# Kernel optimization log

Hardware: AMD Instinct MI355X
Metric: run time of the kernel (lower is better)

Reference implementation:

```python
import jax, jax.numpy as jnp
import numpy as np

LOG_VAR_Q = 0.0
TEMPERATURE = 0.5


def setup_inputs() -> dict:
    key = jax.random.key(0)
    k1, k2, k3 = jax.random.split(key, 3)
    bs, dim_z, W, H, K = 64, 64, 32, 32, 1024
    x = jax.random.normal(k1, (bs, dim_z, W, H), dtype=jnp.float32)
    codebook = jax.random.normal(k2, (K, dim_z), dtype=jnp.float32)
    log_var_q_scalar = jnp.asarray(0.0, dtype=jnp.float32)
    # pre-sampled standard Gumbel noise for the relaxed categorical
    u = jax.random.uniform(k3, (bs * W * H, K), dtype=jnp.float32,
                           minval=1e-6, maxval=1.0 - 1e-6)
    gumbel_noise = -jnp.log(-jnp.log(u))
    return {"x": x, "codebook": codebook,
            "log_var_q_scalar": log_var_q_scalar,
            "gumbel_noise": gumbel_noise}


def reference(x, codebook, log_var_q_scalar, gumbel_noise):
    bs, dim_z, W, H = x.shape
    # [bs, dim_z, W, H] -> [bs*W*H, dim_z]
    x_flat = jnp.transpose(x, (0, 2, 3, 1)).reshape(-1, dim_z)

    var_q = jnp.exp(jnp.asarray(LOG_VAR_Q, x.dtype)) + jnp.exp(log_var_q_scalar)
    precision_q = 1.0 / jnp.clip(var_q, 1e-10)
    w = 0.5 * precision_q  # scalar weight on squared distances

    sq_x = jnp.sum(x_flat * x_flat, axis=-1, keepdims=True)
    sq_c = jnp.sum(codebook * codebook, axis=-1)
    cross = jnp.einsum('nd,kd->nk', x_flat, codebook)
    logit = -w * (sq_x - 2.0 * cross + sq_c)

    log_probs = jax.nn.log_softmax(logit, axis=-1)
    probs = jnp.exp(log_probs)

    # gumbel-softmax relaxed one-hot encodings
    encodings = jax.nn.softmax((logit + gumbel_noise) / TEMPERATURE, axis=-1)

    quantized = jnp.einsum('nk,kd->nd', encodings, codebook)
    quantized = jnp.transpose(quantized.reshape(bs, W, H, dim_z), (0, 3, 1, 2))

    kld_discrete = jnp.sum(probs * log_probs) / bs
    kld_continuous = jnp.mean(jnp.sum(w * (x - quantized) ** 2, axis=(1, 2, 3)))
    return quantized, kld_discrete + kld_continuous
```

## Files before the change

### kernel.cpp

```cpp
#include <hip/hip_runtime.h>
#include <math.h>

#define K_CB 1024
#define D_Z  64
#define MT   16
#define NTOT 65536
#define NBLK (NTOT / MT)

typedef __attribute__((ext_vector_type(8))) short  s16x8;
typedef __attribute__((ext_vector_type(4))) short  s16x4;
typedef __attribute__((ext_vector_type(4))) float  f32x4;

#define WS_CB16  0
#define WS_CBT16 131072
#define WS_NWSQC 262144
#define WS_PART  266240

__device__ __forceinline__ unsigned short f2b(float f) {
  unsigned int u = __float_as_uint(f);
  u += 0x7fffu + ((u >> 16) & 1u);
  return (unsigned short)(u >> 16);
}

__global__ void vq_prep(const float* __restrict__ cb, const float* __restrict__ lvq,
                        unsigned char* __restrict__ wsb) {
  unsigned short* cb16  = (unsigned short*)(wsb + WS_CB16);
  unsigned short* cbT16 = (unsigned short*)(wsb + WS_CBT16);
  float* nwsqc = (float*)(wsb + WS_NWSQC);
  const float w = 0.5f / fmaxf(1.0f + __expf(lvq[0]), 1e-10f);
  const int tid = threadIdx.x;
  const int k  = blockIdx.x * 16 + (tid >> 4);
  const int d0 = (tid & 15) * 4;
  const f32x4 v = *(const f32x4*)(cb + k * D_Z + d0);
  s16x4 b4;
  #pragma unroll
  for (int i = 0; i < 4; i++) b4[i] = (short)f2b(v[i]);
  *(s16x4*)(cb16 + k * D_Z + d0) = b4;
  #pragma unroll
  for (int i = 0; i < 4; i++) cbT16[(d0 + i) * K_CB + k] = (unsigned short)b4[i];
  float s = v[0]*v[0] + v[1]*v[1] + v[2]*v[2] + v[3]*v[3];
  #pragma unroll
  for (int off = 1; off < 16; off <<= 1) s += __shfl_xor(s, off);
  if ((tid & 15) == 0) nwsqc[k] = -w * s;
}

__global__ __launch_bounds__(256, 3)
void vq_main(const float* __restrict__ x, const float* __restrict__ gum,
             const float* __restrict__ lvq, unsigned char* __restrict__ wsb,
             float* __restrict__ out) {
  __shared__ __align__(16) unsigned short xa[1024];
  __shared__ __align__(16) float xs[MT][68];
  __shared__ __align__(16) float sqcs[K_CB];
  __shared__ __align__(16) unsigned short es[MT][1032];
  __shared__ __align__(16) float pstat[4][MT][4];
  __shared__ __align__(16) float s2p[4][MT];
  __shared__ float kldrow[MT];
  __shared__ float wred[4];

  const int tid  = threadIdx.x;
  const int wv   = tid >> 6;
  const int lane = tid & 63;
  const int m16  = lane & 15;
  const int g    = lane >> 4;

  const int blk  = blockIdx.x;
  const int row0 = blk * MT;
  const int bidx = row0 >> 10;
  const int rem0 = row0 & 1023;

  const float w  = 0.5f / fmaxf(1.0f + __expf(lvq[0]), 1e-10f);
  const float w2 = 2.0f * w;

  const unsigned short* cb16  = (const unsigned short*)(wsb + WS_CB16);
  const unsigned short* cbT16 = (const unsigned short*)(wsb + WS_CBT16);
  const float* nwsqc = (const float*)(wsb + WS_NWSQC);

  {
    const int m = tid & 15, db = tid >> 4;
    #pragma unroll
    for (int i = 0; i < 4; i++) {
      const int d = db + 16 * i;
      const float v = x[((bidx * D_Z + d) << 10) + rem0 + m];
      xs[m][d] = v;
      xa[(d >> 5) * 512 + ((d >> 3) & 3) * 128 + m * 8 + (d & 7)] = f2b(v);
    }
    for (int k = tid; k < K_CB; k += 256) sqcs[k] = nwsqc[k];
  }
  __syncthreads();

  f32x4 acc[16];
  #pragma unroll
  for (int t = 0; t < 16; t++) acc[t] = (f32x4){0.f, 0.f, 0.f, 0.f};
  {
    const s16x8 xb0 = *(const s16x8*)(xa + g * 128 + m16 * 8);
    const s16x8 xb1 = *(const s16x8*)(xa + 512 + g * 128 + m16 * 8);
    const unsigned short* ap = cb16 + (wv * 256 + m16) * D_Z + g * 8;
    #pragma unroll
    for (int t = 0; t < 16; t++) {
      const s16x8 a0 = *(const s16x8*)(ap + t * 1024);
      const s16x8 a1 = *(const s16x8*)(ap + t * 1024 + 32);
      acc[t] = __builtin_amdgcn_mfma_f32_16x16x32_bf16(a0, xb0, acc[t], 0, 0, 0);
      acc[t] = __builtin_amdgcn_mfma_f32_16x16x32_bf16(a1, xb1, acc[t], 0, 0, 0);
    }
  }

  float m1 = -3.4e38f;
  #pragma unroll
  for (int t = 0; t < 16; t++) {
    const f32x4 sc = *(const f32x4*)&sqcs[wv * 256 + t * 16 + g * 4];
    #pragma unroll
    for (int r = 0; r < 4; r++) {
      acc[t][r] = fmaf(w2, acc[t][r], sc[r]);
      m1 = fmaxf(m1, acc[t][r]);
    }
  }
  m1 = fmaxf(m1, __shfl_xor(m1, 16));
  m1 = fmaxf(m1, __shfl_xor(m1, 32));
  float s1 = 0.f, Aa = 0.f;
  #pragma unroll
  for (int t = 0; t < 16; t++) {
    #pragma unroll
    for (int r = 0; r < 4; r++) {
      const float u = acc[t][r] - m1;
      const float e = __expf(u);
      s1 += e;
      Aa = fmaf(u, e, Aa);
    }
  }
  s1 += __shfl_xor(s1, 16); s1 += __shfl_xor(s1, 32);
  Aa += __shfl_xor(Aa, 16); Aa += __shfl_xor(Aa, 32);

  float m2 = -3.4e38f;
  const float* gp = gum + (row0 + m16) * K_CB + wv * 256 + g * 4;
  #pragma unroll
  for (int t = 0; t < 16; t++) {
    const f32x4 gv = __builtin_nontemporal_load((const f32x4*)(gp + t * 16));
    #pragma unroll
    for (int r = 0; r < 4; r++) {
      const float z = 2.0f * (acc[t][r] + gv[r]);
      acc[t][r] = z;
      m2 = fmaxf(m2, z);
    }
  }
  m2 = fmaxf(m2, __shfl_xor(m2, 16));
  m2 = fmaxf(m2, __shfl_xor(m2, 32));
  if (g == 0) {
    pstat[wv][m16][0] = m1; pstat[wv][m16][1] = s1;
    pstat[wv][m16][2] = Aa; pstat[wv][m16][3] = m2;
  }
  __syncthreads();

  float M2 = -3.4e38f;
  {
    float M1 = -3.4e38f;
    f32x4 pw[4];
    #pragma unroll
    for (int q = 0; q < 4; q++) {
      pw[q] = *(const f32x4*)&pstat[q][m16][0];
      M1 = fmaxf(M1, pw[q][0]);
      M2 = fmaxf(M2, pw[q][3]);
    }
    float s1g = 0.f, Ag = 0.f;
    #pragma unroll
    for (int q = 0; q < 4; q++) {
      const float dm = pw[q][0] - M1;
      const float c = __expf(dm);
      s1g += c * pw[q][1];
      Ag = fmaf(c, fmaf(dm, pw[q][1], pw[q][2]), Ag);
    }
    if (tid < 16) kldrow[m16] = Ag / s1g - __logf(s1g);
  }

  float s2 = 0.f;
  #pragma unroll
  for (int t = 0; t < 16; t++) {
    s16x4 ev;
    #pragma unroll
    for (int r = 0; r < 4; r++) {
      const float e = __expf(acc[t][r] - M2);
      s2 += e;
      ev[r] = (short)f2b(e);
    }
    *(s16x4*)&es[m16][wv * 256 + t * 16 + g * 4] = ev;
  }
  s2 += __shfl_xor(s2, 16); s2 += __shfl_xor(s2, 32);
  if (g == 0) s2p[wv][m16] = s2;
  __syncthreads();

  const float inv2 = 1.0f / (s2p[0][m16] + s2p[1][m16] + s2p[2][m16] + s2p[3][m16]);
  f32x4 qacc = (f32x4){0.f, 0.f, 0.f, 0.f};
  {
    const unsigned short* a2p = cbT16 + (wv * 16 + m16) * K_CB + g * 8;
    const unsigned short* b2p = &es[m16][g * 8];
    #pragma unroll
    for (int kc = 0; kc < 32; kc++) {
      const s16x8 a2 = *(const s16x8*)(a2p + kc * 32);
      const s16x8 b2 = *(const s16x8*)(b2p + kc * 32);
      qacc = __builtin_amdgcn_mfma_f32_16x16x32_bf16(a2, b2, qacc, 0, 0, 0);
    }
  }

  float kca = 0.f;
  #pragma unroll
  for (int r = 0; r < 4; r++) {
    const int d = wv * 16 + g * 4 + r;
    const float qv = qacc[r] * inv2;
    __builtin_nontemporal_store(qv, out + ((bidx * D_Z + d) << 10) + rem0 + m16);
    const float dx = xs[m16][d] - qv;
    kca = fmaf(dx, dx, kca);
  }
  #pragma unroll
  for (int off = 1; off < 64; off <<= 1) kca += __shfl_xor(kca, off);
  if (lane == 0) wred[wv] = kca;
  __syncthreads();
  if (tid == 0) {
    float tot = w * (wred[0] + wred[1] + wred[2] + wred[3]);
    #pragma unroll
    for (int i = 0; i < MT; i++) tot += kldrow[i];
    ((float*)(wsb + WS_PART))[blk] = tot;
  }
}

__global__ void vq_reduce(const unsigned char* __restrict__ wsb, float* __restrict__ out) {
  __shared__ float red[256];
  const float* part = (const float*)(wsb + WS_PART);
  const int t = threadIdx.x;
  float s = 0.f;
  for (int i = t; i < NBLK; i += 256) s += part[i];
  red[t] = s;
  __syncthreads();
  for (int st = 128; st > 0; st >>= 1) {
    if (t < st) red[t] += red[t + st];
    __syncthreads();
  }
  if (t == 0) out[NTOT * D_Z] = red[0] * (1.0f / 64.0f);
}

extern "C" void kernel_launch(void* const* d_in, const int* in_sizes, int n_in,
                              void* d_out, int out_size, void* d_ws, size_t ws_size,
                              hipStream_t stream) {
  const float* x   = (const float*)d_in[0];
  const float* cb  = (const float*)d_in[1];
  const float* lvq = (const float*)d_in[2];
  const float* gum = (const float*)d_in[3];
  float* out = (float*)d_out;
  unsigned char* wsb = (unsigned char*)d_ws;

  hipLaunchKernelGGL(vq_prep,   dim3(64),   dim3(256), 0, stream, cb, lvq, wsb);
  hipLaunchKernelGGL(vq_main,   dim3(NBLK), dim3(256), 0, stream, x, gum, lvq, wsb, out);
  hipLaunchKernelGGL(vq_reduce, dim3(1),    dim3(256), 0, stream, wsb, out);
}
```

Before: 179.1 us.

## Keep softmax weights in registers and split-K the second GEMM across waves

The second GEMM (encodings × codebook) changes from having each wave cover 16 output dims over all K, read from an LDS bf16 buffer, to having each wave cover its own 256-codebook slice. The exponentials in registers are packed directly into MFMA B-fragments, using a permuted transposed codebook layout (colof) so register order matches. Per-wave partial outputs are then combined in swizzled LDS with per-wave max rescaling, which removes the es staging buffer and one barrier. Other changes: gumbel loads are issued earlier in two batches, the sqc staging in LDS is dropped, the xs fp32 copy is removed, and blocks are remapped for locality. The KL term now uses bf16-rounded x, a small accuracy loss, and the rescaling adds extra LDS traffic.

```diff
diff --git a/kernel.cpp b/kernel.cpp
--- a/kernel.cpp
+++ b/kernel.cpp
@@ -1,4 +1,5 @@
 #include <hip/hip_runtime.h>
+#include <hip/hip_bf16.h>
 #include <math.h>
 
 #define K_CB 1024
@@ -7,12 +8,12 @@
 #define NTOT 65536
 #define NBLK (NTOT / MT)
 
-typedef __attribute__((ext_vector_type(8))) short  s16x8;
-typedef __attribute__((ext_vector_type(4))) short  s16x4;
-typedef __attribute__((ext_vector_type(4))) float  f32x4;
+typedef __attribute__((ext_vector_type(8))) short s16x8;
+typedef __attribute__((ext_vector_type(4))) short s16x4;
+typedef __attribute__((ext_vector_type(4))) float f32x4;
 
 #define WS_CB16  0
-#define WS_CBT16 131072
+#define WS_CBT2  131072
 #define WS_NWSQC 262144
 #define WS_PART  266240
 
@@ -21,11 +22,25 @@
   u += 0x7fffu + ((u >> 16) & 1u);
   return (unsigned short)(u >> 16);
 }
+__device__ __forceinline__ unsigned int pk2b(float lo, float hi) {
+  float2 v; v.x = lo; v.y = hi;
+  __hip_bfloat162 h = __float22bfloat162_rn(v);
+  return *(unsigned int*)&h;
+}
+__device__ __forceinline__ float b2f(unsigned short u) {
+  return __uint_as_float(((unsigned int)u) << 16);
+}
+
+__device__ __forceinline__ int colof(int k) {
+  const int r = k & 255;
+  return (k & ~255) | ((r >> 5) << 5) | (((r >> 2) & 3) << 3)
+       | (((r >> 4) & 1) << 2) | (r & 3);
+}
 
 __global__ void vq_prep(const float* __restrict__ cb, const float* __restrict__ lvq,
                         unsigned char* __restrict__ wsb) {
-  unsigned short* cb16  = (unsigned short*)(wsb + WS_CB16);
-  unsigned short* cbT16 = (unsigned short*)(wsb + WS_CBT16);
+  unsigned short* cb16 = (unsigned short*)(wsb + WS_CB16);
+  unsigned short* cbT2 = (unsigned short*)(wsb + WS_CBT2);
   float* nwsqc = (float*)(wsb + WS_NWSQC);
   const float w = 0.5f / fmaxf(1.0f + __expf(lvq[0]), 1e-10f);
   const int tid = threadIdx.x;
@@ -36,8 +51,9 @@
   #pragma unroll
   for (int i = 0; i < 4; i++) b4[i] = (short)f2b(v[i]);
   *(s16x4*)(cb16 + k * D_Z + d0) = b4;
-  #pragma unroll
-  for (int i = 0; i < 4; i++) cbT16[(d0 + i) * K_CB + k] = (unsigned short)b4[i];
+  const int col = colof(k);
+  #pragma unroll
+  for (int i = 0; i < 4; i++) cbT2[(d0 + i) * K_CB + col] = (unsigned short)b4[i];
   float s = v[0]*v[0] + v[1]*v[1] + v[2]*v[2] + v[3]*v[3];
   #pragma unroll
   for (int off = 1; off < 16; off <<= 1) s += __shfl_xor(s, off);
@@ -48,31 +64,29 @@
 void vq_main(const float* __restrict__ x, const float* __restrict__ gum,
              const float* __restrict__ lvq, unsigned char* __restrict__ wsb,
              float* __restrict__ out) {
-  __shared__ __align__(16) unsigned short xa[1024];
-  __shared__ __align__(16) float xs[MT][68];
-  __shared__ __align__(16) float sqcs[K_CB];
-  __shared__ __align__(16) unsigned short es[MT][1032];
-  __shared__ __align__(16) float pstat[4][MT][4];
-  __shared__ __align__(16) float s2p[4][MT];
-  __shared__ float kldrow[MT];
+  __shared__ __align__(16) unsigned short xa[MT * D_Z];
+  __shared__ __align__(16) float qpart[4][MT][D_Z];
+  __shared__ __align__(16) float st4[4][MT][4];
+  __shared__ __align__(16) float s2s[4][MT];
   __shared__ float wred[4];
 
   const int tid  = threadIdx.x;
-  const int wv   = tid >> 6;
+  const int w    = tid >> 6;
   const int lane = tid & 63;
   const int m16  = lane & 15;
   const int g    = lane >> 4;
-
-  const int blk  = blockIdx.x;
+  const int bid  = blockIdx.x;
+  const int blk  = ((bid & 7) << 9) | (bid >> 3);
   const int row0 = blk * MT;
   const int bidx = row0 >> 10;
   const int rem0 = row0 & 1023;
-
-  const float w  = 0.5f / fmaxf(1.0f + __expf(lvq[0]), 1e-10f);
-  const float w2 = 2.0f * w;
-
-  const unsigned short* cb16  = (const unsigned short*)(wsb + WS_CB16);
-  const unsigned short* cbT16 = (const unsigned short*)(wsb + WS_CBT16);
+  const int kw0  = w << 8;
+
+  const float wq = 0.5f / fmaxf(1.0f + __expf(lvq[0]), 1e-10f);
+  const float w2 = 2.0f * wq;
+
+  const unsigned short* cb16 = (const unsigned short*)(wsb + WS_CB16);
+  const unsigned short* cbT2 = (const unsigned short*)(wsb + WS_CBT2);
   const float* nwsqc = (const float*)(wsb + WS_NWSQC);
 
   {
@@ -81,10 +95,8 @@
     for (int i = 0; i < 4; i++) {
       const int d = db + 16 * i;
       const float v = x[((bidx * D_Z + d) << 10) + rem0 + m];
-      xs[m][d] = v;
       xa[(d >> 5) * 512 + ((d >> 3) & 3) * 128 + m * 8 + (d & 7)] = f2b(v);
     }
-    for (int k = tid; k < K_CB; k += 256) sqcs[k] = nwsqc[k];
   }
   __syncthreads();
 
@@ -94,7 +106,7 @@
   {
     const s16x8 xb0 = *(const s16x8*)(xa + g * 128 + m16 * 8);
     const s16x8 xb1 = *(const s16x8*)(xa + 512 + g * 128 + m16 * 8);
-    const unsigned short* ap = cb16 + (wv * 256 + m16) * D_Z + g * 8;
+    const unsigned short* ap = cb16 + (kw0 + m16) * D_Z + g * 8;
     #pragma unroll
     for (int t = 0; t < 16; t++) {
       const s16x8 a0 = *(const s16x8*)(ap + t * 1024);
@@ -107,21 +119,27 @@
   float m1 = -3.4e38f;
   #pragma unroll
   for (int t = 0; t < 16; t++) {
-    const f32x4 sc = *(const f32x4*)&sqcs[wv * 256 + t * 16 + g * 4];
-    #pragma unroll
-    for (int r = 0; r < 4; r++) {
-      acc[t][r] = fmaf(w2, acc[t][r], sc[r]);
-      m1 = fmaxf(m1, acc[t][r]);
+    const f32x4 nw = *(const f32x4*)(nwsqc + kw0 + t * 16 + g * 4);
+    #pragma unroll
+    for (int i = 0; i < 4; i++) {
+      acc[t][i] = fmaf(w2, acc[t][i], nw[i]);
+      m1 = fmaxf(m1, acc[t][i]);
     }
   }
   m1 = fmaxf(m1, __shfl_xor(m1, 16));
   m1 = fmaxf(m1, __shfl_xor(m1, 32));
+
+  const float* gp = gum + ((size_t)(row0 + m16) << 10) + kw0 + g * 4;
+  f32x4 gA[8];
+  #pragma unroll
+  for (int u = 0; u < 8; u++) gA[u] = *(const f32x4*)(gp + u * 16);
+
   float s1 = 0.f, Aa = 0.f;
   #pragma unroll
   for (int t = 0; t < 16; t++) {
     #pragma unroll
-    for (int r = 0; r < 4; r++) {
-      const float u = acc[t][r] - m1;
+    for (int i = 0; i < 4; i++) {
+      const float u = acc[t][i] - m1;
       const float e = __expf(u);
       s1 += e;
       Aa = fmaf(u, e, Aa);
@@ -131,93 +149,141 @@
   Aa += __shfl_xor(Aa, 16); Aa += __shfl_xor(Aa, 32);
 
   float m2 = -3.4e38f;
-  const float* gp = gum + (row0 + m16) * K_CB + wv * 256 + g * 4;
-  #pragma unroll
-  for (int t = 0; t < 16; t++) {
-    const f32x4 gv = __builtin_nontemporal_load((const f32x4*)(gp + t * 16));
-    #pragma unroll
-    for (int r = 0; r < 4; r++) {
-      const float z = 2.0f * (acc[t][r] + gv[r]);
-      acc[t][r] = z;
+  #pragma unroll
+  for (int u = 0; u < 8; u++) {
+    #pragma unroll
+    for (int i = 0; i < 4; i++) {
+      const float z = 2.0f * (acc[u][i] + gA[u][i]);
+      acc[u][i] = z;
+      m2 = fmaxf(m2, z);
+    }
+  }
+  f32x4 gB[8];
+  #pragma unroll
+  for (int u = 0; u < 8; u++) gB[u] = *(const f32x4*)(gp + (8 + u) * 16);
+  #pragma unroll
+  for (int u = 0; u < 8; u++) {
+    #pragma unroll
+    for (int i = 0; i < 4; i++) {
+      const float z = 2.0f * (acc[8 + u][i] + gB[u][i]);
+      acc[8 + u][i] = z;
       m2 = fmaxf(m2, z);
     }
   }
   m2 = fmaxf(m2, __shfl_xor(m2, 16));
   m2 = fmaxf(m2, __shfl_xor(m2, 32));
   if (g == 0) {
-    pstat[wv][m16][0] = m1; pstat[wv][m16][1] = s1;
-    pstat[wv][m16][2] = Aa; pstat[wv][m16][3] = m2;
+    f32x4 st = {m1, s1, Aa, m2};
+    *(f32x4*)&st4[w][m16][0] = st;
+  }
+
+  float s2 = 0.f;
+  #pragma unroll
+  for (int t = 0; t < 16; t++) {
+    #pragma unroll
+    for (int i = 0; i < 4; i++) {
+      const float e = __expf(acc[t][i] - m2);
+      acc[t][i] = e;
+      s2 += e;
+    }
+  }
+  s2 += __shfl_xor(s2, 16); s2 += __shfl_xor(s2, 32);
+  if (g == 0) s2s[w][m16] = s2;
+
+  s16x8 fr[8];
+  #pragma unroll
+  for (int ks = 0; ks < 8; ks++) {
+    unsigned int q0 = pk2b(acc[2*ks][0],   acc[2*ks][1]);
+    unsigned int q1 = pk2b(acc[2*ks][2],   acc[2*ks][3]);
+    unsigned int q2 = pk2b(acc[2*ks+1][0], acc[2*ks+1][1]);
+    unsigned int q3 = pk2b(acc[2*ks+1][2], acc[2*ks+1][3]);
+    unsigned int wv4[4] = {q0, q1, q2, q3};
+    fr[ks] = *(s16x8*)wv4;
+  }
+
+  f32x4 qp[4];
+  #pragma unroll
+  for (int dt = 0; dt < 4; dt++) qp[dt] = (f32x4){0.f, 0.f, 0.f, 0.f};
+  {
+    const unsigned short* a2base = cbT2 + m16 * K_CB + kw0 + g * 8;
+    #pragma unroll
+    for (int ks = 0; ks < 8; ks++) {
+      #pragma unroll
+      for (int dt = 0; dt < 4; dt++) {
+        const s16x8 a2 = *(const s16x8*)(a2base + dt * 16 * K_CB + ks * 32);
+        qp[dt] = __builtin_amdgcn_mfma_f32_16x16x32_bf16(a2, fr[ks], qp[dt], 0, 0, 0);
+      }
+    }
+  }
+
+  {
+    unsigned char* qb = (unsigned char*)qpart;
+    #pragma unroll
+    for (int dt = 0; dt < 4; dt++) {
+      const int d0 = dt * 16 + g * 4;
+      const int addr = ((w * 16 + m16) * 256 + d0 * 4) ^ ((m16 & 7) << 4);
+      *(f32x4*)(qb + addr) = qp[dt];
+    }
   }
   __syncthreads();
 
-  float M2 = -3.4e38f;
-  {
-    float M1 = -3.4e38f;
-    f32x4 pw[4];
+  {
+    const int m = lane & 15, dgrp = lane >> 4;
+    const int d0 = w * 16 + dgrp * 4;
+    f32x4 sq[4];
+    #pragma unroll
+    for (int q = 0; q < 4; q++) sq[q] = *(const f32x4*)&st4[q][m][0];
+    float M2 = fmaxf(fmaxf(sq[0][3], sq[1][3]), fmaxf(sq[2][3], sq[3][3]));
+    float cw[4], s2g = 0.f;
     #pragma unroll
     for (int q = 0; q < 4; q++) {
-      pw[q] = *(const f32x4*)&pstat[q][m16][0];
-      M1 = fmaxf(M1, pw[q][0]);
-      M2 = fmaxf(M2, pw[q][3]);
-    }
-    float s1g = 0.f, Ag = 0.f;
+      cw[q] = __expf(sq[q][3] - M2);
+      s2g = fmaf(cw[q], s2s[q][m], s2g);
+    }
+    const float inv2 = 1.0f / s2g;
+    f32x4 osum = (f32x4){0.f, 0.f, 0.f, 0.f};
+    const unsigned char* qb = (const unsigned char*)qpart;
     #pragma unroll
     for (int q = 0; q < 4; q++) {
-      const float dm = pw[q][0] - M1;
-      const float c = __expf(dm);
-      s1g += c * pw[q][1];
-      Ag = fmaf(c, fmaf(dm, pw[q][1], pw[q][2]), Ag);
-    }
-    if (tid < 16) kldrow[m16] = Ag / s1g - __logf(s1g);
-  }
-
-  float s2 = 0.f;
-  #pragma unroll
-  for (int t = 0; t < 16; t++) {
-    s16x4 ev;
+      const int addr = ((q * 16 + m) * 256 + d0 * 4) ^ ((m & 7) << 4);
+      const f32x4 p = *(const f32x4*)(qb + addr);
+      #pragma unroll
+      for (int i = 0; i < 4; i++) osum[i] = fmaf(cw[q], p[i], osum[i]);
+    }
+    float kca = 0.f;
+    const s16x4 xb = *(const s16x4*)&xa[(d0 >> 5) * 512 + ((d0 >> 3) & 3) * 128 + m * 8 + (d0 & 7)];
     #pragma unroll
     for (int r = 0; r < 4; r++) {
-      const float e = __expf(acc[t][r] - M2);
-      s2 += e;
-      ev[r] = (short)f2b(e);
-    }
-    *(s16x4*)&es[m16][wv * 256 + t * 16 + g * 4] = ev;
-  }
-  s2 += __shfl_xor(s2, 16); s2 += __shfl_xor(s2, 32);
-  if (g == 0) s2p[wv][m16] = s2;
-  __syncthreads();
-
-  const float inv2 = 1.0f / (s2p[0][m16] + s2p[1][m16] + s2p[2][m16] + s2p[3][m16]);
-  f32x4 qacc = (f32x4){0.f, 0.f, 0.f, 0.f};
-  {
-    const unsigned short* a2p = cbT16 + (wv * 16 + m16) * K_CB + g * 8;
-    const unsigned short* b2p = &es[m16][g * 8];
-    #pragma unroll
-    for (int kc = 0; kc < 32; kc++) {
-      const s16x8 a2 = *(const s16x8*)(a2p + kc * 32);
-      const s16x8 b2 = *(const s16x8*)(b2p + kc * 32);
-      qacc = __builtin_amdgcn_mfma_f32_16x16x32_bf16(a2, b2, qacc, 0, 0, 0);
-    }
-  }
-
-  float kca = 0.f;
-  #pragma unroll
-  for (int r = 0; r < 4; r++) {
-    const int d = wv * 16 + g * 4 + r;
-    const float qv = qacc[r] * inv2;
-    __builtin_nontemporal_store(qv, out + ((bidx * D_Z + d) << 10) + rem0 + m16);
-    const float dx = xs[m16][d] - qv;
-    kca = fmaf(dx, dx, kca);
-  }
-  #pragma unroll
-  for (int off = 1; off < 64; off <<= 1) kca += __shfl_xor(kca, off);
-  if (lane == 0) wred[wv] = kca;
-  __syncthreads();
-  if (tid == 0) {
-    float tot = w * (wred[0] + wred[1] + wred[2] + wred[3]);
-    #pragma unroll
-    for (int i = 0; i < MT; i++) tot += kldrow[i];
-    ((float*)(wsb + WS_PART))[blk] = tot;
+      const int d = d0 + r;
+      const float qv = osum[r] * inv2;
+      out[((bidx * D_Z + d) << 10) + rem0 + m] = qv;
+      const float dx = b2f((unsigned short)xb[r]) - qv;
+      kca = fmaf(dx, dx, kca);
+    }
+    #pragma unroll
+    for (int off = 1; off < 64; off <<= 1) kca += __shfl_xor(kca, off);
+    if (lane == 0) wred[w] = kca;
+
+    float kld = 0.f;
+    if (w == 0) {
+      float M1 = fmaxf(fmaxf(sq[0][0], sq[1][0]), fmaxf(sq[2][0], sq[3][0]));
+      float s1g = 0.f, Ag = 0.f;
+      #pragma unroll
+      for (int q = 0; q < 4; q++) {
+        const float dm = sq[q][0] - M1;
+        const float c  = __expf(dm);
+        s1g += c * sq[q][1];
+        Ag = fmaf(c, fmaf(dm, sq[q][1], sq[q][2]), Ag);
+      }
+      kld = (dgrp == 0) ? (Ag / s1g - __logf(s1g)) : 0.f;
+      #pragma unroll
+      for (int off = 1; off < 64; off <<= 1) kld += __shfl_xor(kld, off);
+    }
+    __syncthreads();
+    if (tid == 0) {
+      const float tot = wq * (wred[0] + wred[1] + wred[2] + wred[3]) + kld;
+      ((float*)(wsb + WS_PART))[blk] = tot;
+    }
   }
 }
 
```

New measurement: 183.2 us. 2.3% more time.
